# Kernel tuning notes

Hardware: AMD Instinct MI355X
Metric: run time of the kernel (lower is better)

Reference implementation:

```python
import jax, jax.numpy as jnp
import numpy as np

N_NODES = 10000
N_EDGES = 640000
D_IN = 128
D_OUT = 128


def setup_inputs() -> dict:
    key = jax.random.key(0)
    k1, k2, k3, k4 = jax.random.split(key, 4)
    nodes = jax.random.normal(k1, (N_NODES, D_IN), dtype=jnp.float32)
    senders = jax.random.randint(k2, (N_EDGES,), 0, N_NODES, dtype=jnp.int32)
    receivers = jax.random.randint(k3, (N_EDGES,), 0, N_NODES, dtype=jnp.int32)
    W = jax.random.normal(k4, (D_IN, D_OUT), dtype=jnp.float32) / np.sqrt(D_IN)
    b = jnp.zeros((D_OUT,), dtype=jnp.float32)
    return {"nodes": nodes, "senders": senders, "receivers": receivers, "W": W, "b": b}


def reference(nodes, senders, receivers, W, b):
    # gather messages from sender nodes: [E, D_IN]
    messages = nodes[senders]
    # scatter-add into receiver nodes: [N, D_IN]
    aggregated = jax.ops.segment_sum(messages, receivers, num_segments=nodes.shape[0])
    # in-degree per receiver node: [N]
    ones = jnp.ones((senders.shape[0],), dtype=nodes.dtype)
    degree = jax.ops.segment_sum(ones, receivers, num_segments=nodes.shape[0])
    degree = jnp.maximum(degree, 1.0)
    aggregated = aggregated / degree[:, None]
    # linear projection: [N, D_OUT]
    new_nodes = aggregated @ W + b
    return new_nodes
```

## Files before the change

### kernel.cpp

```cpp
#include <hip/hip_runtime.h>

#define N_NODES 10000
#define N_EDGES 640000
#define D       128

#define GEMM_BLOCKS 313
#define HB          64
#define CHUNK       10000
#define PAD         256
#define GROUPS      8
#define NODES_PER_GROUP 1250
#define SBPG        128

__device__ inline unsigned bf16pair(float a, float b) {
    unsigned ua = __float_as_uint(a), ub = __float_as_uint(b);
    ua = (ua + 0x7fffu + ((ua >> 16) & 1u)) >> 16;
    ub = (ub + 0x7fffu + ((ub >> 16) & 1u)) >> 16;
    return ua | (ub << 16);
}

union FusedSmem {
    float As[32][132];
    int   cnt[N_NODES];
};

__global__ __launch_bounds__(256) void gemm_hist_kernel(const float* __restrict__ nodes,
                                                        const float* __restrict__ Wm,
                                                        unsigned* __restrict__ Yb,
                                                        const int* __restrict__ senders,
                                                        const int* __restrict__ receivers,
                                                        unsigned* __restrict__ pack,
                                                        int* __restrict__ bcnt) {
    __shared__ FusedSmem sm;
    const int t = threadIdx.x;

    if (blockIdx.x < GEMM_BLOCKS) {
        const int row0 = blockIdx.x * 32;

        for (int i = t; i < 1024; i += 256) {
            int r  = i >> 5;
            int c  = i & 31;
            int gr = row0 + r;
            float4 v = make_float4(0.f, 0.f, 0.f, 0.f);
            if (gr < N_NODES) v = ((const float4*)nodes)[gr * 32 + c];
            *((float4*)&sm.As[r][c * 4]) = v;
        }
        __syncthreads();

        const int tx = t & 15;
        const int ty = t >> 4;
        const int c0 = tx * 8;
        const int r0 = ty * 2;

        float acc[2][8];
#pragma unroll
        for (int i = 0; i < 2; i++)
#pragma unroll
            for (int j = 0; j < 8; j++) acc[i][j] = 0.f;

        const float4* W4 = (const float4*)Wm;
#pragma unroll 4
        for (int k = 0; k < 128; k++) {
            float  a0 = sm.As[r0][k];
            float  a1 = sm.As[r0 + 1][k];
            float4 w0 = W4[k * 32 + tx * 2];
            float4 w1 = W4[k * 32 + tx * 2 + 1];
            float  wv[8] = {w0.x, w0.y, w0.z, w0.w, w1.x, w1.y, w1.z, w1.w};
#pragma unroll
            for (int j = 0; j < 8; j++) {
                acc[0][j] += a0 * wv[j];
                acc[1][j] += a1 * wv[j];
            }
        }

#pragma unroll
        for (int i = 0; i < 2; i++) {
            int gr = row0 + r0 + i;
            if (gr < N_NODES) {
                uint4 o;
                o.x = bf16pair(acc[i][0], acc[i][1]);
                o.y = bf16pair(acc[i][2], acc[i][3]);
                o.z = bf16pair(acc[i][4], acc[i][5]);
                o.w = bf16pair(acc[i][6], acc[i][7]);
                ((uint4*)Yb)[gr * 16 + (c0 >> 3)] = o;
            }
        }
    } else {
        const int b = blockIdx.x - GEMM_BLOCKS;
        for (int n = t; n < N_NODES; n += 256) sm.cnt[n] = 0;
        __syncthreads();
        const int base = b * CHUNK;
        for (int i = t; i < CHUNK; i += 256) {
            int r = receivers[base + i];
            int s = senders[base + i];
            int l = atomicAdd(&sm.cnt[r], 1);
            pack[base + i] = (unsigned)s | ((unsigned)r << 14) | ((unsigned)l << 28);
        }
        __syncthreads();
        int* dst = bcnt + b * N_NODES;
        for (int n = t; n < N_NODES; n += 256) dst[n] = sm.cnt[n];
    }
}

__global__ __launch_bounds__(256) void colscan_kernel(int* __restrict__ bcnt,
                                                      int* __restrict__ deg) {
    const int g = blockIdx.x * 256 + threadIdx.x;
    const int n = g >> 2;
    const int q = g & 3;
    if (n >= N_NODES) return;

    int pre[16];
    int s = 0;
#pragma unroll
    for (int j = 0; j < 16; j++) {
        int v = bcnt[(q * 16 + j) * N_NODES + n];
        pre[j] = s;
        s += v;
    }

    const int lane = threadIdx.x & 63;
    const int gb   = lane & ~3;
    int s0 = __shfl(s, gb + 0);
    int s1 = __shfl(s, gb + 1);
    int s2 = __shfl(s, gb + 2);
    int off = (q > 0 ? s0 : 0) + (q > 1 ? s1 : 0) + (q > 2 ? s2 : 0);

#pragma unroll
    for (int j = 0; j < 16; j++)
        bcnt[(q * 16 + j) * N_NODES + n] = off + pre[j];
    if (q == 3) deg[n] = off + s;
}

__global__ __launch_bounds__(256) void scatter_kernel(const unsigned* __restrict__ pack,
                                                      const int* __restrict__ bcnt,
                                                      int* __restrict__ csr) {
    const int x  = blockIdx.x & 7;
    const int bg = blockIdx.x >> 3;
    const int lo = x * NODES_PER_GROUP;
    const int hi = lo + NODES_PER_GROUP;

    for (int i = bg * 256 + threadIdx.x; i < N_EDGES / 4; i += SBPG * 256) {
        int b = i / (CHUNK / 4);
        const int* pre = bcnt + b * N_NODES;
        uint4 p = ((const uint4*)pack)[i];
#pragma unroll
        for (int q = 0; q < 4; q++) {
            unsigned wd = (q == 0) ? p.x : (q == 1) ? p.y : (q == 2) ? p.z : p.w;
            int r = (int)((wd >> 14) & 0x3fffu);
            if (r >= lo && r < hi) {
                int s = (int)(wd & 0x3fffu);
                int l = (int)(wd >> 28);
                csr[(r << 8) + pre[r] + l] = s;
            }
        }
    }
}

__device__ inline void acc8(float* acc, uint4 v) {
    acc[0] += __uint_as_float(v.x << 16);
    acc[1] += __uint_as_float(v.x & 0xffff0000u);
    acc[2] += __uint_as_float(v.y << 16);
    acc[3] += __uint_as_float(v.y & 0xffff0000u);
    acc[4] += __uint_as_float(v.z << 16);
    acc[5] += __uint_as_float(v.z & 0xffff0000u);
    acc[6] += __uint_as_float(v.w << 16);
    acc[7] += __uint_as_float(v.w & 0xffff0000u);
}

__global__ __launch_bounds__(256) void gather_kernel(const unsigned* __restrict__ Yb,
                                                     const int* __restrict__ deg,
                                                     const int* __restrict__ csr,
                                                     const float* __restrict__ bias,
                                                     float* __restrict__ out) {
    const int t  = threadIdx.x;
    const int d4 = t & 15;
    const int n  = blockIdx.x * 16 + (t >> 4);

    const int dg   = deg[n];
    const int lim  = min(dg, PAD);
    const int base = n << 8;

    float acc[8];
#pragma unroll
    for (int k = 0; k < 8; k++) acc[k] = 0.f;

    const uint4* Y4 = (const uint4*)Yb;

    int j = 0;
    for (; j + 4 <= lim; j += 4) {
        int s0 = csr[base + j];
        int s1 = csr[base + j + 1];
        int s2 = csr[base + j + 2];
        int s3 = csr[base + j + 3];
        uint4 v0 = Y4[s0 * 16 + d4];
        uint4 v1 = Y4[s1 * 16 + d4];
        uint4 v2 = Y4[s2 * 16 + d4];
        uint4 v3 = Y4[s3 * 16 + d4];
        acc8(acc, v0);
        acc8(acc, v1);
        acc8(acc, v2);
        acc8(acc, v3);
    }
    for (; j < lim; j++) {
        int s = csr[base + j];
        acc8(acc, Y4[s * 16 + d4]);
    }

    const float inv = 1.0f / (float)max(dg, 1);
    float4 b0 = ((const float4*)bias)[d4 * 2];
    float4 b1 = ((const float4*)bias)[d4 * 2 + 1];
    float4 o0 = make_float4(acc[0] * inv + b0.x, acc[1] * inv + b0.y,
                            acc[2] * inv + b0.z, acc[3] * inv + b0.w);
    float4 o1 = make_float4(acc[4] * inv + b1.x, acc[5] * inv + b1.y,
                            acc[6] * inv + b1.z, acc[7] * inv + b1.w);
    ((float4*)&out[n * 128 + d4 * 8])[0] = o0;
    ((float4*)&out[n * 128 + d4 * 8])[1] = o1;
}

extern "C" void kernel_launch(void* const* d_in, const int* in_sizes, int n_in,
                              void* d_out, int out_size, void* d_ws, size_t ws_size,
                              hipStream_t stream) {
    const float* nodes     = (const float*)d_in[0];
    const int*   senders   = (const int*)  d_in[1];
    const int*   receivers = (const int*)  d_in[2];
    const float* Wm        = (const float*)d_in[3];
    const float* bias      = (const float*)d_in[4];
    float*       out       = (float*)d_out;

    char*     w    = (char*)d_ws;
    unsigned* Yb   = (unsigned*)(w);
    unsigned* pack = (unsigned*)(w + 2560000);
    int*      bcnt = (int*)(w + 5120000);
    int*      deg  = (int*)(w + 7680000);
    int*      csr  = (int*)(w + 7720448);

    gemm_hist_kernel<<<GEMM_BLOCKS + HB, 256, 0, stream>>>(nodes, Wm, Yb,
                                                           senders, receivers,
                                                           pack, bcnt);
    colscan_kernel  <<<(4 * N_NODES + 255) / 256, 256, 0, stream>>>(bcnt, deg);
    scatter_kernel  <<<GROUPS * SBPG, 256, 0, stream>>>(pack, bcnt, csr);
    gather_kernel   <<<(N_NODES + 15) / 16, 256, 0, stream>>>(Yb, deg, csr, bias, out);
}
```

Baseline: 112.9 us.

## Build padded CSR directly per node range, dropping histogram, scan and scatter kernels

Replaces the histogram/column-scan/scatter pipeline with 64 build blocks, each scanning all edges and claiming a 157-node receiver range. Each block uses shared-memory atomics to assign slots and writes senders straight into the padded CSR, while the GEMM blocks run alongside it in the same launch. This removes two kernel launches and the intermediate pack/bcnt traffic. In exchange, every build block rereads the full 5 MB edge list, so edge reads grow 64x, though these hits likely land in L2/MALL.

```diff
diff --git a/kernel.cpp b/kernel.cpp
--- a/kernel.cpp
+++ b/kernel.cpp
@@ -4,13 +4,11 @@
 #define N_EDGES 640000
 #define D       128
 
-#define GEMM_BLOCKS 313
-#define HB          64
-#define CHUNK       10000
-#define PAD         256
-#define GROUPS      8
-#define NODES_PER_GROUP 1250
-#define SBPG        128
+#define BUILD_BLOCKS 64
+#define NPB          157
+#define GEMM_BLOCKS  313
+#define NBLK         (BUILD_BLOCKS + GEMM_BLOCKS)
+#define PAD          256
 
 __device__ inline unsigned bf16pair(float a, float b) {
     unsigned ua = __float_as_uint(a), ub = __float_as_uint(b);
@@ -21,21 +19,62 @@
 
 union FusedSmem {
     float As[32][132];
-    int   cnt[N_NODES];
+    int   cnt[NPB];
 };
 
-__global__ __launch_bounds__(256) void gemm_hist_kernel(const float* __restrict__ nodes,
-                                                        const float* __restrict__ Wm,
-                                                        unsigned* __restrict__ Yb,
-                                                        const int* __restrict__ senders,
-                                                        const int* __restrict__ receivers,
-                                                        unsigned* __restrict__ pack,
-                                                        int* __restrict__ bcnt) {
+__device__ inline void acc8(float* acc, uint4 v) {
+    acc[0] += __uint_as_float(v.x << 16);
+    acc[1] += __uint_as_float(v.x & 0xffff0000u);
+    acc[2] += __uint_as_float(v.y << 16);
+    acc[3] += __uint_as_float(v.y & 0xffff0000u);
+    acc[4] += __uint_as_float(v.z << 16);
+    acc[5] += __uint_as_float(v.z & 0xffff0000u);
+    acc[6] += __uint_as_float(v.w << 16);
+    acc[7] += __uint_as_float(v.w & 0xffff0000u);
+}
+
+__global__ __launch_bounds__(256) void gemm_build_kernel(
+    const float* __restrict__ nodes, const float* __restrict__ Wm,
+    unsigned* __restrict__ Yb,
+    const int* __restrict__ senders, const int* __restrict__ receivers,
+    int* __restrict__ deg, int* __restrict__ csr)
+{
     __shared__ FusedSmem sm;
     const int t = threadIdx.x;
 
-    if (blockIdx.x < GEMM_BLOCKS) {
-        const int row0 = blockIdx.x * 32;
+    if (blockIdx.x < BUILD_BLOCKS) {
+        const int lo = blockIdx.x * NPB;
+        const int hi = min(lo + NPB, N_NODES);
+
+        for (int i = t; i < NPB; i += 256) sm.cnt[i] = 0;
+        __syncthreads();
+
+        const int4* s4 = (const int4*)senders;
+        const int4* r4 = (const int4*)receivers;
+        for (int i = t; i < N_EDGES / 4; i += 256) {
+            int4 r = r4[i];
+            int4 s = s4[i];
+            if (r.x >= lo && r.x < hi) {
+                int l = atomicAdd(&sm.cnt[r.x - lo], 1);
+                csr[(r.x << 8) + l] = s.x;
+            }
+            if (r.y >= lo && r.y < hi) {
+                int l = atomicAdd(&sm.cnt[r.y - lo], 1);
+                csr[(r.y << 8) + l] = s.y;
+            }
+            if (r.z >= lo && r.z < hi) {
+                int l = atomicAdd(&sm.cnt[r.z - lo], 1);
+                csr[(r.z << 8) + l] = s.z;
+            }
+            if (r.w >= lo && r.w < hi) {
+                int l = atomicAdd(&sm.cnt[r.w - lo], 1);
+                csr[(r.w << 8) + l] = s.w;
+            }
+        }
+        __syncthreads();
+        for (int i = t; lo + i < hi; i += 256) deg[lo + i] = sm.cnt[i];
+    } else {
+        const int row0 = (blockIdx.x - BUILD_BLOCKS) * 32;
 
         for (int i = t; i < 1024; i += 256) {
             int r  = i >> 5;
@@ -49,7 +88,6 @@
 
         const int tx = t & 15;
         const int ty = t >> 4;
-        const int c0 = tx * 8;
         const int r0 = ty * 2;
 
         float acc[2][8];
@@ -82,89 +120,10 @@
                 o.y = bf16pair(acc[i][2], acc[i][3]);
                 o.z = bf16pair(acc[i][4], acc[i][5]);
                 o.w = bf16pair(acc[i][6], acc[i][7]);
-                ((uint4*)Yb)[gr * 16 + (c0 >> 3)] = o;
-            }
-        }
-    } else {
-        const int b = blockIdx.x - GEMM_BLOCKS;
-        for (int n = t; n < N_NODES; n += 256) sm.cnt[n] = 0;
-        __syncthreads();
-        const int base = b * CHUNK;
-        for (int i = t; i < CHUNK; i += 256) {
-            int r = receivers[base + i];
-            int s = senders[base + i];
-            int l = atomicAdd(&sm.cnt[r], 1);
-            pack[base + i] = (unsigned)s | ((unsigned)r << 14) | ((unsigned)l << 28);
-        }
-        __syncthreads();
-        int* dst = bcnt + b * N_NODES;
-        for (int n = t; n < N_NODES; n += 256) dst[n] = sm.cnt[n];
-    }
-}
-
-__global__ __launch_bounds__(256) void colscan_kernel(int* __restrict__ bcnt,
-                                                      int* __restrict__ deg) {
-    const int g = blockIdx.x * 256 + threadIdx.x;
-    const int n = g >> 2;
-    const int q = g & 3;
-    if (n >= N_NODES) return;
-
-    int pre[16];
-    int s = 0;
-#pragma unroll
-    for (int j = 0; j < 16; j++) {
-        int v = bcnt[(q * 16 + j) * N_NODES + n];
-        pre[j] = s;
-        s += v;
-    }
-
-    const int lane = threadIdx.x & 63;
-    const int gb   = lane & ~3;
-    int s0 = __shfl(s, gb + 0);
-    int s1 = __shfl(s, gb + 1);
-    int s2 = __shfl(s, gb + 2);
-    int off = (q > 0 ? s0 : 0) + (q > 1 ? s1 : 0) + (q > 2 ? s2 : 0);
-
-#pragma unroll
-    for (int j = 0; j < 16; j++)
-        bcnt[(q * 16 + j) * N_NODES + n] = off + pre[j];
-    if (q == 3) deg[n] = off + s;
-}
-
-__global__ __launch_bounds__(256) void scatter_kernel(const unsigned* __restrict__ pack,
-                                                      const int* __restrict__ bcnt,
-                                                      int* __restrict__ csr) {
-    const int x  = blockIdx.x & 7;
-    const int bg = blockIdx.x >> 3;
-    const int lo = x * NODES_PER_GROUP;
-    const int hi = lo + NODES_PER_GROUP;
-
-    for (int i = bg * 256 + threadIdx.x; i < N_EDGES / 4; i += SBPG * 256) {
-        int b = i / (CHUNK / 4);
-        const int* pre = bcnt + b * N_NODES;
-        uint4 p = ((const uint4*)pack)[i];
-#pragma unroll
-        for (int q = 0; q < 4; q++) {
-            unsigned wd = (q == 0) ? p.x : (q == 1) ? p.y : (q == 2) ? p.z : p.w;
-            int r = (int)((wd >> 14) & 0x3fffu);
-            if (r >= lo && r < hi) {
-                int s = (int)(wd & 0x3fffu);
-                int l = (int)(wd >> 28);
-                csr[(r << 8) + pre[r] + l] = s;
+                ((uint4*)Yb)[gr * 16 + tx] = o;
             }
         }
     }
-}
-
-__device__ inline void acc8(float* acc, uint4 v) {
-    acc[0] += __uint_as_float(v.x << 16);
-    acc[1] += __uint_as_float(v.x & 0xffff0000u);
-    acc[2] += __uint_as_float(v.y << 16);
-    acc[3] += __uint_as_float(v.y & 0xffff0000u);
-    acc[4] += __uint_as_float(v.z << 16);
-    acc[5] += __uint_as_float(v.z & 0xffff0000u);
-    acc[6] += __uint_as_float(v.w << 16);
-    acc[7] += __uint_as_float(v.w & 0xffff0000u);
 }
 
 __global__ __launch_bounds__(256) void gather_kernel(const unsigned* __restrict__ Yb,
@@ -227,17 +186,12 @@
     const float* bias      = (const float*)d_in[4];
     float*       out       = (float*)d_out;
 
-    char*     w    = (char*)d_ws;
-    unsigned* Yb   = (unsigned*)(w);
-    unsigned* pack = (unsigned*)(w + 2560000);
-    int*      bcnt = (int*)(w + 5120000);
-    int*      deg  = (int*)(w + 7680000);
-    int*      csr  = (int*)(w + 7720448);
+    char*     w   = (char*)d_ws;
+    unsigned* Yb  = (unsigned*)(w);
+    int*      deg = (int*)(w + 2560000);
+    int*      csr = (int*)(w + 2600192);
 
-    gemm_hist_kernel<<<GEMM_BLOCKS + HB, 256, 0, stream>>>(nodes, Wm, Yb,
-                                                           senders, receivers,
-                                                           pack, bcnt);
-    colscan_kernel  <<<(4 * N_NODES + 255) / 256, 256, 0, stream>>>(bcnt, deg);
-    scatter_kernel  <<<GROUPS * SBPG, 256, 0, stream>>>(pack, bcnt, csr);
-    gather_kernel   <<<(N_NODES + 15) / 16, 256, 0, stream>>>(Yb, deg, csr, bias, out);
+    gemm_build_kernel<<<NBLK, 256, 0, stream>>>(nodes, Wm, Yb, senders,
+                                                receivers, deg, csr);
+    gather_kernel<<<(N_NODES + 15) / 16, 256, 0, stream>>>(Yb, deg, csr, bias, out);
 }
```

After: 403.8 us. +257.7%, slower.

## Pack histogram counters as 16-bit pairs and put histogram blocks first

Applied to the files above, without the earlier changes.

The histogram blocks now keep per-node counters as packed 16-bit halves, which halves the shared-memory footprint (about 20KB instead of 40KB) and so allows more resident blocks per CU. Histogram blocks are moved to the front of the grid so the long-running atomic work starts first. The GEMM tile drops from 32 to 16 rows per block with one row per thread, doubling the GEMM block count and removing the bounds checks. In exchange, W is reloaded from global memory by twice as many blocks, and each thread does less arithmetic per W load.

```diff
diff --git a/kernel.cpp b/kernel.cpp
--- a/kernel.cpp
+++ b/kernel.cpp
@@ -4,8 +4,8 @@
 #define N_EDGES 640000
 #define D       128
 
-#define GEMM_BLOCKS 313
 #define HB          64
+#define GEMM_BLOCKS 625
 #define CHUNK       10000
 #define PAD         256
 #define GROUPS      8
@@ -20,9 +20,20 @@
 }
 
 union FusedSmem {
-    float As[32][132];
-    int   cnt[N_NODES];
+    float    As[16][132];
+    unsigned cnt2[N_NODES / 2];
 };
+
+__device__ inline void acc8(float* acc, uint4 v) {
+    acc[0] += __uint_as_float(v.x << 16);
+    acc[1] += __uint_as_float(v.x & 0xffff0000u);
+    acc[2] += __uint_as_float(v.y << 16);
+    acc[3] += __uint_as_float(v.y & 0xffff0000u);
+    acc[4] += __uint_as_float(v.z << 16);
+    acc[5] += __uint_as_float(v.z & 0xffff0000u);
+    acc[6] += __uint_as_float(v.w << 16);
+    acc[7] += __uint_as_float(v.w & 0xffff0000u);
+}
 
 __global__ __launch_bounds__(256) void gemm_hist_kernel(const float* __restrict__ nodes,
                                                         const float* __restrict__ Wm,
@@ -34,71 +45,63 @@
     __shared__ FusedSmem sm;
     const int t = threadIdx.x;
 
-    if (blockIdx.x < GEMM_BLOCKS) {
-        const int row0 = blockIdx.x * 32;
-
-        for (int i = t; i < 1024; i += 256) {
-            int r  = i >> 5;
-            int c  = i & 31;
-            int gr = row0 + r;
-            float4 v = make_float4(0.f, 0.f, 0.f, 0.f);
-            if (gr < N_NODES) v = ((const float4*)nodes)[gr * 32 + c];
-            *((float4*)&sm.As[r][c * 4]) = v;
-        }
-        __syncthreads();
-
-        const int tx = t & 15;
-        const int ty = t >> 4;
-        const int c0 = tx * 8;
-        const int r0 = ty * 2;
-
-        float acc[2][8];
-#pragma unroll
-        for (int i = 0; i < 2; i++)
-#pragma unroll
-            for (int j = 0; j < 8; j++) acc[i][j] = 0.f;
-
-        const float4* W4 = (const float4*)Wm;
-#pragma unroll 4
-        for (int k = 0; k < 128; k++) {
-            float  a0 = sm.As[r0][k];
-            float  a1 = sm.As[r0 + 1][k];
-            float4 w0 = W4[k * 32 + tx * 2];
-            float4 w1 = W4[k * 32 + tx * 2 + 1];
-            float  wv[8] = {w0.x, w0.y, w0.z, w0.w, w1.x, w1.y, w1.z, w1.w};
-#pragma unroll
-            for (int j = 0; j < 8; j++) {
-                acc[0][j] += a0 * wv[j];
-                acc[1][j] += a1 * wv[j];
-            }
-        }
-
-#pragma unroll
-        for (int i = 0; i < 2; i++) {
-            int gr = row0 + r0 + i;
-            if (gr < N_NODES) {
-                uint4 o;
-                o.x = bf16pair(acc[i][0], acc[i][1]);
-                o.y = bf16pair(acc[i][2], acc[i][3]);
-                o.z = bf16pair(acc[i][4], acc[i][5]);
-                o.w = bf16pair(acc[i][6], acc[i][7]);
-                ((uint4*)Yb)[gr * 16 + (c0 >> 3)] = o;
-            }
-        }
-    } else {
-        const int b = blockIdx.x - GEMM_BLOCKS;
-        for (int n = t; n < N_NODES; n += 256) sm.cnt[n] = 0;
+    if (blockIdx.x < HB) {
+        const int b = blockIdx.x;
+        for (int n = t; n < N_NODES / 2; n += 256) sm.cnt2[n] = 0;
         __syncthreads();
         const int base = b * CHUNK;
         for (int i = t; i < CHUNK; i += 256) {
             int r = receivers[base + i];
             int s = senders[base + i];
-            int l = atomicAdd(&sm.cnt[r], 1);
-            pack[base + i] = (unsigned)s | ((unsigned)r << 14) | ((unsigned)l << 28);
+            unsigned sh  = (unsigned)(r & 1) * 16u;
+            unsigned old = atomicAdd(&sm.cnt2[r >> 1], 1u << sh);
+            unsigned l   = (old >> sh) & 0xffffu;
+            pack[base + i] = (unsigned)s | ((unsigned)r << 14) | (l << 28);
         }
         __syncthreads();
         int* dst = bcnt + b * N_NODES;
-        for (int n = t; n < N_NODES; n += 256) dst[n] = sm.cnt[n];
+        for (int n = t; n < N_NODES; n += 256)
+            dst[n] = (int)((sm.cnt2[n >> 1] >> ((unsigned)(n & 1) * 16u)) & 0xffffu);
+    } else {
+        const int row0 = (blockIdx.x - HB) * 16;
+
+        for (int i = t; i < 512; i += 256) {
+            int r = i >> 5;
+            int c = i & 31;
+            *((float4*)&sm.As[r][c * 4]) = ((const float4*)nodes)[(row0 + r) * 32 + c];
+        }
+        __syncthreads();
+
+        const int tx  = t & 15;
+        const int ty  = t >> 4;
+        const int row = row0 + ty;
+
+        float acc[8];
+#pragma unroll
+        for (int j = 0; j < 8; j++) acc[j] = 0.f;
+
+        const float4* W4 = (const float4*)Wm;
+#pragma unroll 4
+        for (int k = 0; k < 128; k++) {
+            float  a0 = sm.As[ty][k];
+            float4 w0 = W4[k * 32 + tx * 2];
+            float4 w1 = W4[k * 32 + tx * 2 + 1];
+            acc[0] += a0 * w0.x;
+            acc[1] += a0 * w0.y;
+            acc[2] += a0 * w0.z;
+            acc[3] += a0 * w0.w;
+            acc[4] += a0 * w1.x;
+            acc[5] += a0 * w1.y;
+            acc[6] += a0 * w1.z;
+            acc[7] += a0 * w1.w;
+        }
+
+        uint4 o;
+        o.x = bf16pair(acc[0], acc[1]);
+        o.y = bf16pair(acc[2], acc[3]);
+        o.z = bf16pair(acc[4], acc[5]);
+        o.w = bf16pair(acc[6], acc[7]);
+        ((uint4*)Yb)[row * 16 + tx] = o;
     }
 }
 
@@ -154,17 +157,6 @@
             }
         }
     }
-}
-
-__device__ inline void acc8(float* acc, uint4 v) {
-    acc[0] += __uint_as_float(v.x << 16);
-    acc[1] += __uint_as_float(v.x & 0xffff0000u);
-    acc[2] += __uint_as_float(v.y << 16);
-    acc[3] += __uint_as_float(v.y & 0xffff0000u);
-    acc[4] += __uint_as_float(v.z << 16);
-    acc[5] += __uint_as_float(v.z & 0xffff0000u);
-    acc[6] += __uint_as_float(v.w << 16);
-    acc[7] += __uint_as_float(v.w & 0xffff0000u);
 }
 
 __global__ __launch_bounds__(256) void gather_kernel(const unsigned* __restrict__ Yb,
@@ -234,7 +226,7 @@
     int*      deg  = (int*)(w + 7680000);
     int*      csr  = (int*)(w + 7720448);
 
-    gemm_hist_kernel<<<GEMM_BLOCKS + HB, 256, 0, stream>>>(nodes, Wm, Yb,
+    gemm_hist_kernel<<<HB + GEMM_BLOCKS, 256, 0, stream>>>(nodes, Wm, Yb,
                                                            senders, receivers,
                                                            pack, bcnt);
     colscan_kernel  <<<(4 * N_NODES + 255) / 256, 256, 0, stream>>>(bcnt, deg);
```

Result: slower. 119.8 us (+6.1%).
